# Kernel tuning notes

Hardware: AMD Instinct MI355X
Metric: run time of the kernel (lower is better)

## Reference

```python
import jax, jax.numpy as jnp
import numpy as np

HIDDEN = 32


def setup_inputs() -> dict:
    key = jax.random.key(0)
    ks = jax.random.split(key, 8)
    B, T, I = 1024, 512, 64
    s_ih = 1.0 / np.sqrt(HIDDEN)
    return {
        "x": jax.random.normal(ks[0], (B, T, I), dtype=jnp.float32),
        "h0": jnp.zeros((1, B, HIDDEN), dtype=jnp.float32),
        "W_ih": jax.random.uniform(ks[1], (HIDDEN, I), jnp.float32, -s_ih, s_ih),
        "b_ih": jax.random.uniform(ks[2], (HIDDEN,), jnp.float32, -s_ih, s_ih),
        "W_hh": jax.random.uniform(ks[3], (HIDDEN, HIDDEN), jnp.float32, -s_ih, s_ih),
        "b_hh": jax.random.uniform(ks[4], (HIDDEN,), jnp.float32, -s_ih, s_ih),
        "W_out": jax.random.uniform(ks[5], (1, HIDDEN), jnp.float32, -s_ih, s_ih),
        "b_out": jax.random.uniform(ks[6], (1,), jnp.float32, -s_ih, s_ih),
    }


def reference(x, h0, W_ih, b_ih, W_hh, b_hh, W_out, b_out):
    # x: [B, T, I]; h0: [1, B, H] (num_layers=1)
    # Precompute input contribution for all timesteps in one GEMM: [B, T, H]
    x_proj = jnp.einsum("bti,hi->bth", x, W_ih) + b_ih

    def step(h, xt):  # h: [B, H], xt: [B, H]
        h_new = jnp.tanh(xt + h @ W_hh.T + b_hh)
        return h_new, h_new

    h_last, r_out_t = jax.lax.scan(step, h0[0], jnp.swapaxes(x_proj, 0, 1))
    r_out = jnp.swapaxes(r_out_t, 0, 1)  # [B, T, H]
    # Per-timestep Linear(32 -> 1), batched as one GEMM: [B, T, 1]
    outs = r_out @ W_out.T + b_out
    return outs, h_last[None]
```

## Files before the change

kernel.cpp:

```cpp
#include <hip/hip_runtime.h>

#define Bc 1024
#define Tc 512
#define Ic 64
#define Hc 32
#define XP 516
#define LOG2E2 2.8853900817779268f

typedef __bf16 bf16x8 __attribute__((ext_vector_type(8)));
typedef __bf16 bf16x4 __attribute__((ext_vector_type(4)));
typedef float  f32x4  __attribute__((ext_vector_type(4)));

__device__ inline bf16x8 to_bf16x8(float4 u0, float4 u1) {
    bf16x8 t;
    t[0] = (__bf16)u0.x; t[1] = (__bf16)u0.y; t[2] = (__bf16)u0.z; t[3] = (__bf16)u0.w;
    t[4] = (__bf16)u1.x; t[5] = (__bf16)u1.y; t[6] = (__bf16)u1.z; t[7] = (__bf16)u1.w;
    return t;
}
__device__ inline bf16x8 to_bf16x8s(float4 u0, float4 u1, float s) {
    bf16x8 t;
    t[0] = (__bf16)(u0.x*s); t[1] = (__bf16)(u0.y*s); t[2] = (__bf16)(u0.z*s); t[3] = (__bf16)(u0.w*s);
    t[4] = (__bf16)(u1.x*s); t[5] = (__bf16)(u1.y*s); t[6] = (__bf16)(u1.z*s); t[7] = (__bf16)(u1.w*s);
    return t;
}


#define FMIX_LO(acc, hw, wf)                                                  \
    asm("v_fma_mix_f32 %0, %1, %2, %0 op_sel:[0,0,0] op_sel_hi:[1,0,0]"       \
        : "+v"(acc) : "v"(hw), "v"(wf));
#define FMIX_HI(acc, hw, wf)                                                  \
    asm("v_fma_mix_f32 %0, %1, %2, %0 op_sel:[1,0,0] op_sel_hi:[1,0,0]"       \
        : "+v"(acc) : "v"(hw), "v"(wf));

#define STEP(xval, uu)                                                        \
    {                                                                         \
        hbuf[half][h] = rv;                                                   \
        __builtin_amdgcn_wave_barrier();                                      \
        const uint4 Ha = hq[0], Hb = hq[1], Hc2 = hq[2], Hd2 = hq[3];         \
        float a0 = (xval) + biasc, a1 = 0.f, a2 = 0.f, a3 = 0.f;              \
        FMIX_LO(a0, Ha.x, w0.x)  FMIX_HI(a1, Ha.x, w0.y)                      \
        FMIX_LO(a2, Ha.y, w0.z)  FMIX_HI(a3, Ha.y, w0.w)                      \
        FMIX_LO(a0, Ha.z, w1.x)  FMIX_HI(a1, Ha.z, w1.y)                      \
        FMIX_LO(a2, Ha.w, w1.z)  FMIX_HI(a3, Ha.w, w1.w)                      \
        FMIX_LO(a0, Hb.x, w2.x)  FMIX_HI(a1, Hb.x, w2.y)                      \
        FMIX_LO(a2, Hb.y, w2.z)  FMIX_HI(a3, Hb.y, w2.w)                      \
        FMIX_LO(a0, Hb.z, w3.x)  FMIX_HI(a1, Hb.z, w3.y)                      \
        FMIX_LO(a2, Hb.w, w3.z)  FMIX_HI(a3, Hb.w, w3.w)                      \
        FMIX_LO(a0, Hc2.x, w4.x) FMIX_HI(a1, Hc2.x, w4.y)                     \
        FMIX_LO(a2, Hc2.y, w4.z) FMIX_HI(a3, Hc2.y, w4.w)                     \
        FMIX_LO(a0, Hc2.z, w5.x) FMIX_HI(a1, Hc2.z, w5.y)                     \
        FMIX_LO(a2, Hc2.w, w5.z) FMIX_HI(a3, Hc2.w, w5.w)                     \
        FMIX_LO(a0, Hd2.x, w6.x) FMIX_HI(a1, Hd2.x, w6.y)                     \
        FMIX_LO(a2, Hd2.y, w6.z) FMIX_HI(a3, Hd2.y, w6.w)                     \
        FMIX_LO(a0, Hd2.z, w7.x) FMIX_HI(a1, Hd2.z, w7.y)                     \
        FMIX_LO(a2, Hd2.w, w7.z) FMIX_HI(a3, Hd2.w, w7.w)                     \
        const float a_ = (a0 + a1) + (a2 + a3);                               \
        const float p_ = __builtin_amdgcn_exp2f(a_);                          \
        rr = __builtin_amdgcn_rcpf(p_ + 1.0f);                                \
        rv = (_Float16)rr;                                                    \
        pbuf[half][uu][h] = fmaf(rr, w2o, wo);                                \
        __builtin_amdgcn_wave_barrier();                                      \
    }

#define CVT4(dst, src)                                                        \
    dst.x = (float)(src)[0]; dst.y = (float)(src)[1];                         \
    dst.z = (float)(src)[2]; dst.w = (float)(src)[3];

#define TILE_LOAD(Xn, bb, lt)                                                 \
    do {                                                                      \
        const float* xp_ =                                                    \
            x + ((size_t)(b0 + (bb)) * Tc + (lt) * 16 + m) * Ic + q * 8;      \
        Xn##0 = ((const float4*)xp_)[0];                                      \
        Xn##1 = ((const float4*)xp_)[1];                                      \
        Xn##2 = ((const float4*)(xp_ + 32))[0];                               \
        Xn##3 = ((const float4*)(xp_ + 32))[1];                               \
    } while (0)

#define TILE_MFMA(Xn, bb, lt)                                                 \
    do {                                                                      \
        const bf16x8 A0_ = to_bf16x8(Xn##0, Xn##1);                           \
        const bf16x8 A1_ = to_bf16x8(Xn##2, Xn##3);                           \
        f32x4 ac0 = {0.f, 0.f, 0.f, 0.f};                                     \
        f32x4 ac1 = {0.f, 0.f, 0.f, 0.f};                                     \
        ac0 = __builtin_amdgcn_mfma_f32_16x16x32_bf16(A0_, Bf[0][0], ac0, 0, 0, 0); \
        ac0 = __builtin_amdgcn_mfma_f32_16x16x32_bf16(A1_, Bf[0][1], ac0, 0, 0, 0); \
        ac1 = __builtin_amdgcn_mfma_f32_16x16x32_bf16(A0_, Bf[1][0], ac1, 0, 0, 0); \
        ac1 = __builtin_amdgcn_mfma_f32_16x16x32_bf16(A1_, Bf[1][1], ac1, 0, 0, 0); \
        bf16x4 p0_, p1_;                                                      \
        p0_[0] = (__bf16)(ac0[0] + bias0); p0_[1] = (__bf16)(ac0[1] + bias0); \
        p0_[2] = (__bf16)(ac0[2] + bias0); p0_[3] = (__bf16)(ac0[3] + bias0); \
        p1_[0] = (__bf16)(ac1[0] + bias1); p1_[1] = (__bf16)(ac1[1] + bias1); \
        p1_[2] = (__bf16)(ac1[2] + bias1); p1_[3] = (__bf16)(ac1[3] + bias1); \
        *(bf16x4*)&xq[bb][m][(lt) * 16 + q * 4]      = p0_;                   \
        *(bf16x4*)&xq[bb][m + 16][(lt) * 16 + q * 4] = p1_;                   \
    } while (0)

__global__ __launch_bounds__(64) void fused_rnn_kernel(
    const float* __restrict__ x, const float* __restrict__ Wih,
    const float* __restrict__ bih, const float* __restrict__ h0,
    const float* __restrict__ Whh, const float* __restrict__ bhh,
    const float* __restrict__ Wout, const float* __restrict__ bout,
    float* __restrict__ out)
{
    __shared__ __bf16   xq[2][Hc][XP];
    __shared__ _Float16 hbuf[2][32];
    __shared__ float    pbuf[2][16][34];

    const int lane = threadIdx.x;
    const int half = lane >> 5;
    const int h    = lane & 31;
    const int m    = lane & 15;
    const int q    = lane >> 4;
    const int b0   = blockIdx.x * 2;

    bf16x8 Bf[2][2];
#pragma unroll
    for (int nh = 0; nh < 2; ++nh)
#pragma unroll
        for (int kh = 0; kh < 2; ++kh) {
            const float* wp = Wih + (m + 16 * nh) * Ic + q * 8 + kh * 32;
            Bf[nh][kh] = to_bf16x8s(((const float4*)wp)[0],
                                    ((const float4*)wp)[1], LOG2E2);
        }
    const float bias0 = bih[m] * LOG2E2;
    const float bias1 = bih[m + 16] * LOG2E2;

    const float4* wrow = (const float4*)(Whh + h * Hc);
    float4 t0 = wrow[0], t1 = wrow[1], t2 = wrow[2], t3 = wrow[3],
           t4 = wrow[4], t5 = wrow[5], t6 = wrow[6], t7 = wrow[7];
    const float rsum =
        (((t0.x + t0.y) + (t0.z + t0.w)) + ((t1.x + t1.y) + (t1.z + t1.w))) +
        (((t2.x + t2.y) + (t2.z + t2.w)) + ((t3.x + t3.y) + (t3.z + t3.w))) +
        (((t4.x + t4.y) + (t4.z + t4.w)) + ((t5.x + t5.y) + (t5.z + t5.w))) +
        (((t6.x + t6.y) + (t6.z + t6.w)) + ((t7.x + t7.y) + (t7.z + t7.w)));
    const float cw = -2.0f * LOG2E2;
    float4 w0, w1, w2, w3, w4, w5, w6, w7;
    w0.x = t0.x*cw; w0.y = t0.y*cw; w0.z = t0.z*cw; w0.w = t0.w*cw;
    w1.x = t1.x*cw; w1.y = t1.y*cw; w1.z = t1.z*cw; w1.w = t1.w*cw;
    w2.x = t2.x*cw; w2.y = t2.y*cw; w2.z = t2.z*cw; w2.w = t2.w*cw;
    w3.x = t3.x*cw; w3.y = t3.y*cw; w3.z = t3.z*cw; w3.w = t3.w*cw;
    w4.x = t4.x*cw; w4.y = t4.y*cw; w4.z = t4.z*cw; w4.w = t4.w*cw;
    w5.x = t5.x*cw; w5.y = t5.y*cw; w5.z = t5.z*cw; w5.w = t5.w*cw;
    w6.x = t6.x*cw; w6.y = t6.y*cw; w6.z = t6.z*cw; w6.w = t6.w*cw;
    w7.x = t7.x*cw; w7.y = t7.y*cw; w7.z = t7.z*cw; w7.w = t7.w*cw;
    const float biasc = (bhh[h] + rsum) * LOG2E2;
    const float wo  = Wout[h];
    const float w2o = -2.0f * wo;
    const float bo  = bout[0];

    float rr = fmaf(-0.5f, h0[(size_t)(b0 + half) * Hc + h], 0.5f);
    _Float16 rv = (_Float16)rr;
    float* orow = out + (size_t)(b0 + half) * Tc;

    float4 Xa0, Xa1, Xa2, Xa3, Xb0, Xb1, Xb2, Xb3;
    TILE_LOAD(Xa, 0, 0);  TILE_LOAD(Xb, 1, 0);
    TILE_MFMA(Xa, 0, 0);  TILE_MFMA(Xb, 1, 0);
    TILE_LOAD(Xa, 0, 1);  TILE_LOAD(Xb, 1, 1);
    TILE_MFMA(Xa, 0, 1);  TILE_MFMA(Xb, 1, 1);
    TILE_LOAD(Xa, 0, 2);  TILE_LOAD(Xb, 1, 2);
    __builtin_amdgcn_wave_barrier();

    const __bf16* xrow = &xq[half][h][0];
    const uint4*  hq   = (const uint4*)&hbuf[half][0];

    bf16x4 r0 = *(const bf16x4*)(xrow + 0), r1 = *(const bf16x4*)(xrow + 4),
           r2 = *(const bf16x4*)(xrow + 8), r3 = *(const bf16x4*)(xrow + 12);
    float4 q0, q1, q2, q3;
    CVT4(q0, r0) CVT4(q1, r1) CVT4(q2, r2) CVT4(q3, r3)

#pragma unroll 1
    for (int tb = 0; tb < Tc / 16; ++tb) {
        const int tbn = (tb + 1 < Tc / 16) ? tb + 1 : tb;
        const __bf16* nx = xrow + tbn * 16;
        const bf16x4 m0 = *(const bf16x4*)(nx + 0),
                     m1 = *(const bf16x4*)(nx + 4),
                     m2 = *(const bf16x4*)(nx + 8),
                     m3 = *(const bf16x4*)(nx + 12);

        if (tb + 2 < Tc / 16) { TILE_MFMA(Xa, 0, tb + 2); TILE_MFMA(Xb, 1, tb + 2); }
        if (tb + 3 < Tc / 16) { TILE_LOAD(Xa, 0, tb + 3); TILE_LOAD(Xb, 1, tb + 3); }

        STEP(q0.x, 0)  STEP(q0.y, 1)  STEP(q0.z, 2)  STEP(q0.w, 3)
        STEP(q1.x, 4)  STEP(q1.y, 5)  STEP(q1.z, 6)  STEP(q1.w, 7)
        STEP(q2.x, 8)  STEP(q2.y, 9)  STEP(q2.z, 10) STEP(q2.w, 11)
        STEP(q3.x, 12) STEP(q3.y, 13) STEP(q3.z, 14) STEP(q3.w, 15)

        __builtin_amdgcn_wave_barrier();

        if (h < 16) {
            const float2* pr = (const float2*)pbuf[half][h];
            float2 sa = pr[0], sb = pr[1];
#pragma unroll
            for (int mm = 2; mm < 16; mm += 2) {
                sa.x += pr[mm].x;     sa.y += pr[mm].y;
                sb.x += pr[mm + 1].x; sb.y += pr[mm + 1].y;
            }
            orow[tb * 16 + h] = ((sa.x + sb.x) + (sa.y + sb.y)) + bo;
        }
        __builtin_amdgcn_wave_barrier();

        CVT4(q0, m0) CVT4(q1, m1) CVT4(q2, m2) CVT4(q3, m3)
    }

    out[(size_t)Bc * Tc + (size_t)(b0 + half) * Hc + h] = fmaf(-2.0f, rr, 1.0f);
}

extern "C" void kernel_launch(void* const* d_in, const int* in_sizes, int n_in,
                              void* d_out, int out_size, void* d_ws, size_t ws_size,
                              hipStream_t stream) {
    const float* x    = (const float*)d_in[0];
    const float* h0   = (const float*)d_in[1];
    const float* Wih  = (const float*)d_in[2];
    const float* bih  = (const float*)d_in[3];
    const float* Whh  = (const float*)d_in[4];
    const float* bhh  = (const float*)d_in[5];
    const float* Wout = (const float*)d_in[6];
    const float* bout = (const float*)d_in[7];
    float* out = (float*)d_out;

    fused_rnn_kernel<<<Bc / 2, 64, 0, stream>>>(x, Wih, bih, h0, Whh, bhh,
                                                Wout, bout, out);
}
```

Baseline: 244.4 us.

## Broadcast hidden state via permlane16 swap and DPP rotations instead of LDS

Replaces the per-step LDS round trip for the hidden state (write to hbuf, wave barrier, four vector LDS reads) with in-register lane exchange. A permlane16_swap packs pairs of fp16 hidden values, and a tree of DPP row rotations gives each lane all 32 values. W_hh is pre-permuted per lane to match the rotated order, so the matvec uses fdot2 on half2 pairs instead of v_fma_mix. This removes LDS latency from the serial recurrence critical path, at the cost of 16 dependent DPP moves per step and weights held in fp16.

After: 229.1 us. -6.2%, faster.

```diff
diff --git a/kernel.cpp b/kernel.cpp
--- a/kernel.cpp
+++ b/kernel.cpp
@@ -10,6 +10,8 @@
 typedef __bf16 bf16x8 __attribute__((ext_vector_type(8)));
 typedef __bf16 bf16x4 __attribute__((ext_vector_type(4)));
 typedef float  f32x4  __attribute__((ext_vector_type(4)));
+typedef _Float16 half2v __attribute__((ext_vector_type(2)));
+typedef unsigned uint2v __attribute__((ext_vector_type(2)));
 
 __device__ inline bf16x8 to_bf16x8(float4 u0, float4 u1) {
     bf16x8 t;
@@ -25,41 +27,60 @@
 }
 
 
-#define FMIX_LO(acc, hw, wf)                                                  \
-    asm("v_fma_mix_f32 %0, %1, %2, %0 op_sel:[0,0,0] op_sel_hi:[1,0,0]"       \
-        : "+v"(acc) : "v"(hw), "v"(wf));
-#define FMIX_HI(acc, hw, wf)                                                  \
-    asm("v_fma_mix_f32 %0, %1, %2, %0 op_sel:[1,0,0] op_sel_hi:[1,0,0]"       \
-        : "+v"(acc) : "v"(hw), "v"(wf));
+#if __has_builtin(__builtin_amdgcn_permlane16_swap)
+#define PLSWAP(A, B)                                                          \
+    { uint2v _t = __builtin_amdgcn_permlane16_swap((A), (B), false, false);   \
+      (A) = _t[0]; (B) = _t[1]; }
+#else
+#define PLSWAP(A, B)                                                          \
+    asm("s_nop 1\n\tv_permlane16_swap_b32 %0, %1" : "+v"(A), "+v"(B));
+#endif
+
+#define RORD(dst, src, N)                                                     \
+    dst = (unsigned)__builtin_amdgcn_mov_dpp((int)(src), 0x120 + (N), 0xF, 0xF, false);
+
+#if __has_builtin(__builtin_amdgcn_fdot2)
+#define FDOT(g, W, a)                                                         \
+    __builtin_amdgcn_fdot2(__builtin_bit_cast(half2v, (unsigned)(g)), (W), (a), false)
+#else
+__device__ inline float fdot2_emul(unsigned g, half2v w, float a) {
+    half2v v = __builtin_bit_cast(half2v, g);
+    a = fmaf((float)v[0], (float)w[0], a);
+    return fmaf((float)v[1], (float)w[1], a);
+}
+#define FDOT(g, W, a) fdot2_emul((g), (W), (a))
+#endif
+
+#define GATHER(cc)                                                            \
+    unsigned _r0 = (cc), _r1 = (cc);                                          \
+    PLSWAP(_r0, _r1);                                                         \
+    const unsigned _pt = psel ? _r0 : _r1;                                    \
+    unsigned g0 = (_pt << 16) | ((cc) & 0xFFFFu);                             \
+    unsigned g1, g2, g3, g4, g5, g6, g7, g8, g9, g10, g11, g12, g13, g14, g15;\
+    RORD(g1, g0, 8)                                                           \
+    RORD(g2, g0, 4)  RORD(g3, g1, 4)                                          \
+    RORD(g4, g0, 2)  RORD(g5, g1, 2)  RORD(g6, g2, 2)  RORD(g7, g3, 2)        \
+    RORD(g8, g0, 1)  RORD(g9, g1, 1)  RORD(g10, g2, 1) RORD(g11, g3, 1)       \
+    RORD(g12, g4, 1) RORD(g13, g5, 1) RORD(g14, g6, 1) RORD(g15, g7, 1)
 
 #define STEP(xval, uu)                                                        \
     {                                                                         \
-        hbuf[half][h] = rv;                                                   \
-        __builtin_amdgcn_wave_barrier();                                      \
-        const uint4 Ha = hq[0], Hb = hq[1], Hc2 = hq[2], Hd2 = hq[3];         \
+        GATHER(c)                                                             \
         float a0 = (xval) + biasc, a1 = 0.f, a2 = 0.f, a3 = 0.f;              \
-        FMIX_LO(a0, Ha.x, w0.x)  FMIX_HI(a1, Ha.x, w0.y)                      \
-        FMIX_LO(a2, Ha.y, w0.z)  FMIX_HI(a3, Ha.y, w0.w)                      \
-        FMIX_LO(a0, Ha.z, w1.x)  FMIX_HI(a1, Ha.z, w1.y)                      \
-        FMIX_LO(a2, Ha.w, w1.z)  FMIX_HI(a3, Ha.w, w1.w)                      \
-        FMIX_LO(a0, Hb.x, w2.x)  FMIX_HI(a1, Hb.x, w2.y)                      \
-        FMIX_LO(a2, Hb.y, w2.z)  FMIX_HI(a3, Hb.y, w2.w)                      \
-        FMIX_LO(a0, Hb.z, w3.x)  FMIX_HI(a1, Hb.z, w3.y)                      \
-        FMIX_LO(a2, Hb.w, w3.z)  FMIX_HI(a3, Hb.w, w3.w)                      \
-        FMIX_LO(a0, Hc2.x, w4.x) FMIX_HI(a1, Hc2.x, w4.y)                     \
-        FMIX_LO(a2, Hc2.y, w4.z) FMIX_HI(a3, Hc2.y, w4.w)                     \
-        FMIX_LO(a0, Hc2.z, w5.x) FMIX_HI(a1, Hc2.z, w5.y)                     \
-        FMIX_LO(a2, Hc2.w, w5.z) FMIX_HI(a3, Hc2.w, w5.w)                     \
-        FMIX_LO(a0, Hd2.x, w6.x) FMIX_HI(a1, Hd2.x, w6.y)                     \
-        FMIX_LO(a2, Hd2.y, w6.z) FMIX_HI(a3, Hd2.y, w6.w)                     \
-        FMIX_LO(a0, Hd2.z, w7.x) FMIX_HI(a1, Hd2.z, w7.y)                     \
-        FMIX_LO(a2, Hd2.w, w7.z) FMIX_HI(a3, Hd2.w, w7.w)                     \
+        a0 = FDOT(g0,  W0,  a0); a1 = FDOT(g1,  W1,  a1);                     \
+        a2 = FDOT(g2,  W2,  a2); a3 = FDOT(g3,  W3,  a3);                     \
+        a0 = FDOT(g4,  W4,  a0); a1 = FDOT(g5,  W5,  a1);                     \
+        a2 = FDOT(g6,  W6,  a2); a3 = FDOT(g7,  W7,  a3);                     \
+        a0 = FDOT(g8,  W8,  a0); a1 = FDOT(g9,  W9,  a1);                     \
+        a2 = FDOT(g10, W10, a2); a3 = FDOT(g11, W11, a3);                     \
+        a0 = FDOT(g12, W12, a0); a1 = FDOT(g13, W13, a1);                     \
+        a2 = FDOT(g14, W14, a2); a3 = FDOT(g15, W15, a3);                     \
         const float a_ = (a0 + a1) + (a2 + a3);                               \
         const float p_ = __builtin_amdgcn_exp2f(a_);                          \
         rr = __builtin_amdgcn_rcpf(p_ + 1.0f);                                \
-        rv = (_Float16)rr;                                                    \
+        const _Float16 rv_ = (_Float16)rr;                                    \
+        c = (unsigned)__builtin_bit_cast(unsigned short, rv_);                \
         pbuf[half][uu][h] = fmaf(rr, w2o, wo);                                \
-        __builtin_amdgcn_wave_barrier();                                      \
     }
 
 #define CVT4(dst, src)                                                        \
@@ -103,7 +124,6 @@
     float* __restrict__ out)
 {
     __shared__ __bf16   xq[2][Hc][XP];
-    __shared__ _Float16 hbuf[2][32];
     __shared__ float    pbuf[2][16][34];
 
     const int lane = threadIdx.x;
@@ -125,31 +145,53 @@
     const float bias0 = bih[m] * LOG2E2;
     const float bias1 = bih[m + 16] * LOG2E2;
 
-    const float4* wrow = (const float4*)(Whh + h * Hc);
-    float4 t0 = wrow[0], t1 = wrow[1], t2 = wrow[2], t3 = wrow[3],
-           t4 = wrow[4], t5 = wrow[5], t6 = wrow[6], t7 = wrow[7];
+    unsigned ch = (unsigned)h;
+    unsigned d0_ = ch, d1_ = ch;
+    PLSWAP(d0_, d1_);
+    const bool psel = ((d0_ & 0xFFFFu) == (unsigned)(h ^ 16));
+    const unsigned part0 = psel ? d0_ : d1_;
+    unsigned s0 = (part0 << 16) | ch;
+    unsigned s1, s2, s3, s4, s5, s6, s7, s8, s9, s10, s11, s12, s13, s14, s15;
+    RORD(s1, s0, 8)
+    RORD(s2, s0, 4)  RORD(s3, s1, 4)
+    RORD(s4, s0, 2)  RORD(s5, s1, 2)  RORD(s6, s2, 2)  RORD(s7, s3, 2)
+    RORD(s8, s0, 1)  RORD(s9, s1, 1)  RORD(s10, s2, 1) RORD(s11, s3, 1)
+    RORD(s12, s4, 1) RORD(s13, s5, 1) RORD(s14, s6, 1) RORD(s15, s7, 1)
+
+    const float cw = -2.0f * LOG2E2;
+    const float* wr = Whh + h * Hc;
+#define MKW(Wk, sk)                                                           \
+    half2v Wk;                                                                \
+    {                                                                         \
+        const unsigned il_ = (sk) & 0xFFFFu, ih_ = (sk) >> 16;                \
+        Wk[0] = (_Float16)(wr[il_] * cw);                                     \
+        Wk[1] = (_Float16)(wr[ih_] * cw);                                     \
+    }
+    MKW(W0, s0)   MKW(W1, s1)   MKW(W2, s2)   MKW(W3, s3)
+    MKW(W4, s4)   MKW(W5, s5)   MKW(W6, s6)   MKW(W7, s7)
+    MKW(W8, s8)   MKW(W9, s9)   MKW(W10, s10) MKW(W11, s11)
+    MKW(W12, s12) MKW(W13, s13) MKW(W14, s14) MKW(W15, s15)
+#undef MKW
+
+    const float4* wrow = (const float4*)wr;
+    const float4 t0 = wrow[0], t1 = wrow[1], t2 = wrow[2], t3 = wrow[3],
+                 t4 = wrow[4], t5 = wrow[5], t6 = wrow[6], t7 = wrow[7];
     const float rsum =
         (((t0.x + t0.y) + (t0.z + t0.w)) + ((t1.x + t1.y) + (t1.z + t1.w))) +
         (((t2.x + t2.y) + (t2.z + t2.w)) + ((t3.x + t3.y) + (t3.z + t3.w))) +
         (((t4.x + t4.y) + (t4.z + t4.w)) + ((t5.x + t5.y) + (t5.z + t5.w))) +
         (((t6.x + t6.y) + (t6.z + t6.w)) + ((t7.x + t7.y) + (t7.z + t7.w)));
-    const float cw = -2.0f * LOG2E2;
-    float4 w0, w1, w2, w3, w4, w5, w6, w7;
-    w0.x = t0.x*cw; w0.y = t0.y*cw; w0.z = t0.z*cw; w0.w = t0.w*cw;
-    w1.x = t1.x*cw; w1.y = t1.y*cw; w1.z = t1.z*cw; w1.w = t1.w*cw;
-    w2.x = t2.x*cw; w2.y = t2.y*cw; w2.z = t2.z*cw; w2.w = t2.w*cw;
-    w3.x = t3.x*cw; w3.y = t3.y*cw; w3.z = t3.z*cw; w3.w = t3.w*cw;
-    w4.x = t4.x*cw; w4.y = t4.y*cw; w4.z = t4.z*cw; w4.w = t4.w*cw;
-    w5.x = t5.x*cw; w5.y = t5.y*cw; w5.z = t5.z*cw; w5.w = t5.w*cw;
-    w6.x = t6.x*cw; w6.y = t6.y*cw; w6.z = t6.z*cw; w6.w = t6.w*cw;
-    w7.x = t7.x*cw; w7.y = t7.y*cw; w7.z = t7.z*cw; w7.w = t7.w*cw;
     const float biasc = (bhh[h] + rsum) * LOG2E2;
     const float wo  = Wout[h];
     const float w2o = -2.0f * wo;
     const float bo  = bout[0];
 
     float rr = fmaf(-0.5f, h0[(size_t)(b0 + half) * Hc + h], 0.5f);
-    _Float16 rv = (_Float16)rr;
+    {
+        const _Float16 rv0 = (_Float16)rr;
+        ch = (unsigned)__builtin_bit_cast(unsigned short, rv0);
+    }
+    unsigned c = ch;
     float* orow = out + (size_t)(b0 + half) * Tc;
 
     float4 Xa0, Xa1, Xa2, Xa3, Xb0, Xb1, Xb2, Xb3;
@@ -158,10 +200,9 @@
     TILE_LOAD(Xa, 0, 1);  TILE_LOAD(Xb, 1, 1);
     TILE_MFMA(Xa, 0, 1);  TILE_MFMA(Xb, 1, 1);
     TILE_LOAD(Xa, 0, 2);  TILE_LOAD(Xb, 1, 2);
-    __builtin_amdgcn_wave_barrier();
+    __syncthreads();
 
     const __bf16* xrow = &xq[half][h][0];
-    const uint4*  hq   = (const uint4*)&hbuf[half][0];
 
     bf16x4 r0 = *(const bf16x4*)(xrow + 0), r1 = *(const bf16x4*)(xrow + 4),
            r2 = *(const bf16x4*)(xrow + 8), r3 = *(const bf16x4*)(xrow + 12);
```
